# Kernel tuning notes

Measured on AMD Instinct MI355X. Metric: run time of the kernel, lower is better.

The kernel has to match this reference:

```python
import jax, jax.numpy as jnp
import numpy as np

FFT_SIZE = 1024
FRAME_LEN = 256   # stft is called with frame_length = hop_size = 256
FRAME_STEP = 128  # frame_length // 2 (stft default)
N_BINS = FFT_SIZE // 2 + 1
EPS = 1e-8
W_LOG = 1.0
W_LIN = 1.0


def _dft_weights():
    # periodic hann window (scipy get_window(..., fftbins=True))
    n = jnp.arange(FRAME_LEN, dtype=jnp.float32)
    win = 0.5 - 0.5 * jnp.cos(2.0 * jnp.pi * n / FRAME_LEN)
    lp = (FFT_SIZE - FRAME_LEN) // 2
    win = jnp.pad(win, (lp, FFT_SIZE - FRAME_LEN - lp))  # center-pad to n_fft
    # DFT matrix entries exp(-2*pi*i*k*f/n): use exact integer phase mod n_fft
    k = jnp.arange(FFT_SIZE, dtype=jnp.int32)[:, None]
    f = jnp.arange(N_BINS, dtype=jnp.int32)[None, :]
    theta = (-2.0 * jnp.pi / FFT_SIZE) * ((k * f) % FFT_SIZE).astype(jnp.float32)
    w_re = (jnp.cos(theta) * win[:, None])[:, None, :]  # [n_fft, 1, n_bins] (HIO)
    w_im = (jnp.sin(theta) * win[:, None])[:, None, :]
    return w_re, w_im


def _stft_mag(x, w_re, w_im):
    # pad='end' -> pad (0, n_fft - 1) along time
    sig = jnp.pad(x[:, :, None], ((0, 0), (0, FFT_SIZE - 1), (0, 0)))
    dn = ('NHC', 'HIO', 'NHC')
    re = jax.lax.conv_general_dilated(sig, w_re, [FRAME_STEP], 'VALID', dimension_numbers=dn)
    im = jax.lax.conv_general_dilated(sig, w_im, [FRAME_STEP], 'VALID', dimension_numbers=dn)
    # original indexes x_stft[-1]: magnitude of the LAST batch element only
    return jnp.sqrt(jnp.maximum(re[-1] ** 2 + im[-1] ** 2, EPS))  # [frames, n_bins]


def _loss(inp, tgt):
    w_re, w_im = _dft_weights()
    x_mag = _stft_mag(inp, w_re, w_im)
    y_mag = _stft_mag(tgt, w_re, w_im)
    log_mag = jnp.mean(jnp.abs(jnp.log(x_mag) - jnp.log(y_mag)))  # log_eps=0, log_fac=1, L1
    lin_mag = jnp.mean(jnp.abs(x_mag - y_mag))
    return W_LOG * log_mag + W_LIN * lin_mag  # w_sc=0, w_phs=0; 'mean' reduction on scalar is identity


def setup_inputs() -> dict:
    key = jax.random.key(0)
    k1, k2 = jax.random.split(key)
    B, T = 8, 524288
    return {
        'input': jax.random.normal(k1, (B, T), dtype=jnp.float32),
        'target': jax.random.normal(k2, (B, T), dtype=jnp.float32),
    }


def reference(input, target):
    return _loss(input, target)
```

## Files before the change

### kernel.cpp

```cpp
#include <hip/hip_runtime.h>
#include <hip/hip_bf16.h>


#define T_LEN    524288
#define WIN_OFF  384
#define EPSQ     1e-8f
#define INV_N    (1.0f / (4096.0f * 513.0f))
#define A2PI_1024 6.1359231515425647e-3f
#define A2PI_256  2.4543692606170259e-2f

typedef __attribute__((ext_vector_type(8))) __bf16 bf16x8;
typedef __attribute__((ext_vector_type(4))) float  f32x4;

union bfbits { __hip_bfloat16 hb; __bf16 b; unsigned short u; };
static __device__ __forceinline__ __bf16 f2bf(float f) {
    bfbits t; t.hb = __float2bfloat16(f); return t.b;
}

__global__ void prep(const float* __restrict__ x, const float* __restrict__ y,
                     __bf16* __restrict__ xb, __bf16* __restrict__ yb,
                     __bf16* __restrict__ bre, __bf16* __restrict__ bim)
{
    const int tid  = threadIdx.x;
    const int lane = tid & 63;
    const int wid  = blockIdx.x * 4 + (tid >> 6);

    if (wid < 4096) {
        const int sig = wid >> 11;
        const int chunk = wid & 2047;
        const int ft = chunk >> 3;
        const int kk = chunk & 7;
        const float* src = sig ? y : x;
        __bf16*      dst = sig ? yb : xb;
        const int frame = ft * 16 + (lane & 15);
        const int base  = frame * 128 + WIN_OFF + kk * 32 + (lane >> 4) * 8;
        bf16x8 v;
        if (base + 7 < T_LEN) {
            const float4 a0 = *(const float4*)(src + base);
            const float4 a1 = *(const float4*)(src + base + 4);
            v[0]=f2bf(a0.x); v[1]=f2bf(a0.y); v[2]=f2bf(a0.z); v[3]=f2bf(a0.w);
            v[4]=f2bf(a1.x); v[5]=f2bf(a1.y); v[6]=f2bf(a1.z); v[7]=f2bf(a1.w);
        } else {
            #pragma unroll
            for (int j = 0; j < 8; ++j) {
                const int idx = base + j;
                v[j] = f2bf(idx < T_LEN ? src[idx] : 0.f);
            }
        }
        *(bf16x8*)(dst + (size_t)chunk * 512 + lane * 8) = v;
    } else if (wid < 4096 + 256) {
        const int i  = wid - 4096;
        const int bt = i >> 3;
        const int kk = i & 7;
        const int bin = bt * 16 + (lane & 15);
        const int k0  = kk * 32 + (lane >> 4) * 8;
        bf16x8 vr, vi;
        #pragma unroll
        for (int j = 0; j < 8; ++j) {
            const int k = k0 + j;
            const float win = 0.5f - 0.5f * __cosf(A2PI_256 * (float)k);
            const int phase = ((WIN_OFF + k) * bin) & 1023;
            float s, c;
            __sincosf(-A2PI_1024 * (float)phase, &s, &c);
            vr[j] = f2bf(c * win);
            vi[j] = f2bf(s * win);
        }
        const size_t off = (size_t)i * 512 + lane * 8;
        *(bf16x8*)(bre + off) = vr;
        *(bf16x8*)(bim + off) = vi;
    }
}

__launch_bounds__(256, 4)
__global__ void stft_main(const __bf16* __restrict__ xb, const __bf16* __restrict__ yb,
                          const __bf16* __restrict__ bre, const __bf16* __restrict__ bim,
                          const float* __restrict__ x, const float* __restrict__ y,
                          float* __restrict__ partials)
{
    const int tid  = threadIdx.x;
    const int mb   = blockIdx.x & 127;
    const int nb   = blockIdx.x >> 7;

    const int lane = tid & 63;
    const int wv   = tid >> 6;
    const int wr   = wv >> 1;
    const int wc   = wv & 1;

    const int ft  = mb * 2 + wr;
    const int bt0 = nb * 4 + wc * 2;

    const __bf16* pax = xb  + (size_t)ft  * 4096 + lane * 8;
    const __bf16* pay = yb  + (size_t)ft  * 4096 + lane * 8;
    const __bf16* pr0 = bre + (size_t)bt0 * 4096 + lane * 8;
    const __bf16* pi0 = bim + (size_t)bt0 * 4096 + lane * 8;
    const __bf16* pr1 = pr0 + 4096;
    const __bf16* pi1 = pi0 + 4096;

    f32x4 axr[2], axi[2], ayr[2], ayi[2];
    #pragma unroll
    for (int ni = 0; ni < 2; ++ni) {
        axr[ni] = (f32x4)0.f; axi[ni] = (f32x4)0.f;
        ayr[ni] = (f32x4)0.f; ayi[ni] = (f32x4)0.f;
    }

    #pragma unroll 2
    for (int kk = 0; kk < 8; ++kk) {
        const int ko = kk * 512;
        const bf16x8 fax  = *(const bf16x8*)(pax + ko);
        const bf16x8 fay  = *(const bf16x8*)(pay + ko);
        const bf16x8 fbr0 = *(const bf16x8*)(pr0 + ko);
        const bf16x8 fbi0 = *(const bf16x8*)(pi0 + ko);
        const bf16x8 fbr1 = *(const bf16x8*)(pr1 + ko);
        const bf16x8 fbi1 = *(const bf16x8*)(pi1 + ko);

        axr[0] = __builtin_amdgcn_mfma_f32_16x16x32_bf16(fax, fbr0, axr[0], 0, 0, 0);
        axi[0] = __builtin_amdgcn_mfma_f32_16x16x32_bf16(fax, fbi0, axi[0], 0, 0, 0);
        ayr[0] = __builtin_amdgcn_mfma_f32_16x16x32_bf16(fay, fbr0, ayr[0], 0, 0, 0);
        ayi[0] = __builtin_amdgcn_mfma_f32_16x16x32_bf16(fay, fbi0, ayi[0], 0, 0, 0);
        axr[1] = __builtin_amdgcn_mfma_f32_16x16x32_bf16(fax, fbr1, axr[1], 0, 0, 0);
        axi[1] = __builtin_amdgcn_mfma_f32_16x16x32_bf16(fax, fbi1, axi[1], 0, 0, 0);
        ayr[1] = __builtin_amdgcn_mfma_f32_16x16x32_bf16(fay, fbr1, ayr[1], 0, 0, 0);
        ayi[1] = __builtin_amdgcn_mfma_f32_16x16x32_bf16(fay, fbi1, ayi[1], 0, 0, 0);
    }

    float sum = 0.f;
    #pragma unroll
    for (int ni = 0; ni < 2; ++ni)
        #pragma unroll
        for (int r = 0; r < 4; ++r) {
            const float xr = axr[ni][r], xi = axi[ni][r];
            const float yr = ayr[ni][r], yi = ayi[ni][r];
            const float xm = sqrtf(fmaxf(xr * xr + xi * xi, EPSQ));
            const float ym = sqrtf(fmaxf(yr * yr + yi * yi, EPSQ));
            sum += fabsf(__logf(xm) - __logf(ym)) + fabsf(xm - ym);
        }

    {
        float w4[4];
        #pragma unroll
        for (int j = 0; j < 4; ++j) {
            const int m = lane * 4 + j;
            const float win = 0.5f - 0.5f * __cosf(A2PI_256 * (float)m);
            w4[j] = (m & 1) ? -win : win;
        }
        const int frame = blockIdx.x * 4 + wv;
        const int base  = frame * 128 + WIN_OFF + lane * 4;
        float xr, yr;
        if (frame < 4092) {
            const float4 xv = *(const float4*)(x + base);
            const float4 yv = *(const float4*)(y + base);
            xr = xv.x * w4[0] + xv.y * w4[1] + xv.z * w4[2] + xv.w * w4[3];
            yr = yv.x * w4[0] + yv.y * w4[1] + yv.z * w4[2] + yv.w * w4[3];
        } else {
            xr = 0.f; yr = 0.f;
            #pragma unroll
            for (int j = 0; j < 4; ++j) {
                const int idx = base + j;
                if (idx < T_LEN) {
                    xr = fmaf(x[idx], w4[j], xr);
                    yr = fmaf(y[idx], w4[j], yr);
                }
            }
        }
        #pragma unroll
        for (int off = 32; off > 0; off >>= 1) {
            xr += __shfl_xor(xr, off, 64);
            yr += __shfl_xor(yr, off, 64);
        }
        if (lane == 0) {
            const float xm = sqrtf(fmaxf(xr * xr, EPSQ));
            const float ym = sqrtf(fmaxf(yr * yr, EPSQ));
            sum += fabsf(__logf(xm) - __logf(ym)) + fabsf(xm - ym);
        }
    }

    #pragma unroll
    for (int off = 32; off > 0; off >>= 1)
        sum += __shfl_down(sum, off, 64);

    __shared__ float red_s[4];
    if (lane == 0) red_s[wv] = sum;
    __syncthreads();
    if (tid == 0)
        partials[blockIdx.x] = red_s[0] + red_s[1] + red_s[2] + red_s[3];
}

__global__ void reduce_partials(const float* __restrict__ partials,
                                float* __restrict__ out)
{
    const int tid = threadIdx.x;
    float s = partials[tid] + partials[tid + 256]
            + partials[tid + 512] + partials[tid + 768];
    #pragma unroll
    for (int off = 32; off > 0; off >>= 1)
        s += __shfl_down(s, off, 64);

    __shared__ float red[4];
    if ((tid & 63) == 0) red[tid >> 6] = s;
    __syncthreads();
    if (tid == 0)
        out[0] = (red[0] + red[1] + red[2] + red[3]) * INV_N;
}

extern "C" void kernel_launch(void* const* d_in, const int* in_sizes, int n_in,
                              void* d_out, int out_size, void* d_ws, size_t ws_size,
                              hipStream_t stream) {
    const float* input  = (const float*)d_in[0];
    const float* target = (const float*)d_in[1];
    const float* x = input  + (size_t)7 * T_LEN;
    const float* y = target + (size_t)7 * T_LEN;

    char* ws = (char*)d_ws;
    __bf16* wsBre  = (__bf16*)(ws);
    __bf16* wsBim  = (__bf16*)(ws + 262144);
    __bf16* wsXb   = (__bf16*)(ws + 524288);
    __bf16* wsYb   = (__bf16*)(ws + 524288 + 2097152);
    float*  wsPart = (float*) (ws + 524288 + 4194304);

    prep<<<1088, 256, 0, stream>>>(x, y, wsXb, wsYb, wsBre, wsBim);
    stft_main<<<1024, 256, 0, stream>>>(wsXb, wsYb, wsBre, wsBim, x, y, wsPart);
    reduce_partials<<<1, 256, 0, stream>>>(wsPart, (float*)d_out);
}
```

Baseline: 24.24 us.

## Double per-wave frame tiles and fold final reduction into last-block atomic

Each wave now computes a 2x2 grid of 16x16 MFMA tiles (two frame tiles by two bin tiles), which halves the grid to 512 blocks and reuses each loaded fragment across twice as many MFMAs. The separate reduce_partials launch is removed: blocks publish partials with release stores, bump an atomic counter (reset in prep), and the last block sums all partials and writes the output. This is meant to cut global fragment traffic and one kernel launch. In exchange it raises register pressure (32 accumulators, occupancy hint dropped) and leaves fewer blocks to fill the GPU.

```diff
diff --git a/kernel.cpp b/kernel.cpp
--- a/kernel.cpp
+++ b/kernel.cpp
@@ -8,6 +8,7 @@
 #define INV_N    (1.0f / (4096.0f * 513.0f))
 #define A2PI_1024 6.1359231515425647e-3f
 #define A2PI_256  2.4543692606170259e-2f
+#define NBLK     512
 
 typedef __attribute__((ext_vector_type(8))) __bf16 bf16x8;
 typedef __attribute__((ext_vector_type(4))) float  f32x4;
@@ -19,11 +20,14 @@
 
 __global__ void prep(const float* __restrict__ x, const float* __restrict__ y,
                      __bf16* __restrict__ xb, __bf16* __restrict__ yb,
-                     __bf16* __restrict__ bre, __bf16* __restrict__ bim)
+                     __bf16* __restrict__ bre, __bf16* __restrict__ bim,
+                     unsigned* __restrict__ counter)
 {
     const int tid  = threadIdx.x;
     const int lane = tid & 63;
     const int wid  = blockIdx.x * 4 + (tid >> 6);
+
+    if (blockIdx.x == 0 && tid == 0) *counter = 0u;
 
     if (wid < 4096) {
         const int sig = wid >> 11;
@@ -71,69 +75,76 @@
     }
 }
 
-__launch_bounds__(256, 4)
+__launch_bounds__(256)
 __global__ void stft_main(const __bf16* __restrict__ xb, const __bf16* __restrict__ yb,
                           const __bf16* __restrict__ bre, const __bf16* __restrict__ bim,
                           const float* __restrict__ x, const float* __restrict__ y,
-                          float* __restrict__ partials)
+                          float* __restrict__ partials, unsigned* __restrict__ counter,
+                          float* __restrict__ out)
 {
     const int tid  = threadIdx.x;
-    const int mb   = blockIdx.x & 127;
-    const int nb   = blockIdx.x >> 7;
+    const int mb   = blockIdx.x & 63;
+    const int nb   = blockIdx.x >> 6;
 
     const int lane = tid & 63;
     const int wv   = tid >> 6;
     const int wr   = wv >> 1;
     const int wc   = wv & 1;
 
-    const int ft  = mb * 2 + wr;
+    const int ft0 = mb * 4 + wr * 2;
     const int bt0 = nb * 4 + wc * 2;
 
-    const __bf16* pax = xb  + (size_t)ft  * 4096 + lane * 8;
-    const __bf16* pay = yb  + (size_t)ft  * 4096 + lane * 8;
-    const __bf16* pr0 = bre + (size_t)bt0 * 4096 + lane * 8;
-    const __bf16* pi0 = bim + (size_t)bt0 * 4096 + lane * 8;
-    const __bf16* pr1 = pr0 + 4096;
-    const __bf16* pi1 = pi0 + 4096;
-
-    f32x4 axr[2], axi[2], ayr[2], ayi[2];
+    const __bf16* pax0 = xb  + (size_t)ft0 * 4096 + lane * 8;
+    const __bf16* pay0 = yb  + (size_t)ft0 * 4096 + lane * 8;
+    const __bf16* pbr0 = bre + (size_t)bt0 * 4096 + lane * 8;
+    const __bf16* pbi0 = bim + (size_t)bt0 * 4096 + lane * 8;
+
+    f32x4 axr[2][2], axi[2][2], ayr[2][2], ayi[2][2];
     #pragma unroll
-    for (int ni = 0; ni < 2; ++ni) {
-        axr[ni] = (f32x4)0.f; axi[ni] = (f32x4)0.f;
-        ayr[ni] = (f32x4)0.f; ayi[ni] = (f32x4)0.f;
-    }
+    for (int mi = 0; mi < 2; ++mi)
+        #pragma unroll
+        for (int ni = 0; ni < 2; ++ni) {
+            axr[mi][ni] = (f32x4)0.f; axi[mi][ni] = (f32x4)0.f;
+            ayr[mi][ni] = (f32x4)0.f; ayi[mi][ni] = (f32x4)0.f;
+        }
 
     #pragma unroll 2
     for (int kk = 0; kk < 8; ++kk) {
         const int ko = kk * 512;
-        const bf16x8 fax  = *(const bf16x8*)(pax + ko);
-        const bf16x8 fay  = *(const bf16x8*)(pay + ko);
-        const bf16x8 fbr0 = *(const bf16x8*)(pr0 + ko);
-        const bf16x8 fbi0 = *(const bf16x8*)(pi0 + ko);
-        const bf16x8 fbr1 = *(const bf16x8*)(pr1 + ko);
-        const bf16x8 fbi1 = *(const bf16x8*)(pi1 + ko);
-
-        axr[0] = __builtin_amdgcn_mfma_f32_16x16x32_bf16(fax, fbr0, axr[0], 0, 0, 0);
-        axi[0] = __builtin_amdgcn_mfma_f32_16x16x32_bf16(fax, fbi0, axi[0], 0, 0, 0);
-        ayr[0] = __builtin_amdgcn_mfma_f32_16x16x32_bf16(fay, fbr0, ayr[0], 0, 0, 0);
-        ayi[0] = __builtin_amdgcn_mfma_f32_16x16x32_bf16(fay, fbi0, ayi[0], 0, 0, 0);
-        axr[1] = __builtin_amdgcn_mfma_f32_16x16x32_bf16(fax, fbr1, axr[1], 0, 0, 0);
-        axi[1] = __builtin_amdgcn_mfma_f32_16x16x32_bf16(fax, fbi1, axi[1], 0, 0, 0);
-        ayr[1] = __builtin_amdgcn_mfma_f32_16x16x32_bf16(fay, fbr1, ayr[1], 0, 0, 0);
-        ayi[1] = __builtin_amdgcn_mfma_f32_16x16x32_bf16(fay, fbi1, ayi[1], 0, 0, 0);
+        bf16x8 fax[2], fay[2], fbr[2], fbi[2];
+        fax[0] = *(const bf16x8*)(pax0 + ko);
+        fax[1] = *(const bf16x8*)(pax0 + ko + 4096);
+        fay[0] = *(const bf16x8*)(pay0 + ko);
+        fay[1] = *(const bf16x8*)(pay0 + ko + 4096);
+        fbr[0] = *(const bf16x8*)(pbr0 + ko);
+        fbr[1] = *(const bf16x8*)(pbr0 + ko + 4096);
+        fbi[0] = *(const bf16x8*)(pbi0 + ko);
+        fbi[1] = *(const bf16x8*)(pbi0 + ko + 4096);
+
+        #pragma unroll
+        for (int mi = 0; mi < 2; ++mi)
+            #pragma unroll
+            for (int ni = 0; ni < 2; ++ni) {
+                axr[mi][ni] = __builtin_amdgcn_mfma_f32_16x16x32_bf16(fax[mi], fbr[ni], axr[mi][ni], 0, 0, 0);
+                axi[mi][ni] = __builtin_amdgcn_mfma_f32_16x16x32_bf16(fax[mi], fbi[ni], axi[mi][ni], 0, 0, 0);
+                ayr[mi][ni] = __builtin_amdgcn_mfma_f32_16x16x32_bf16(fay[mi], fbr[ni], ayr[mi][ni], 0, 0, 0);
+                ayi[mi][ni] = __builtin_amdgcn_mfma_f32_16x16x32_bf16(fay[mi], fbi[ni], ayi[mi][ni], 0, 0, 0);
+            }
     }
 
     float sum = 0.f;
     #pragma unroll
-    for (int ni = 0; ni < 2; ++ni)
-        #pragma unroll
-        for (int r = 0; r < 4; ++r) {
-            const float xr = axr[ni][r], xi = axi[ni][r];
-            const float yr = ayr[ni][r], yi = ayi[ni][r];
-            const float xm = sqrtf(fmaxf(xr * xr + xi * xi, EPSQ));
-            const float ym = sqrtf(fmaxf(yr * yr + yi * yi, EPSQ));
-            sum += fabsf(__logf(xm) - __logf(ym)) + fabsf(xm - ym);
-        }
+    for (int mi = 0; mi < 2; ++mi)
+        #pragma unroll
+        for (int ni = 0; ni < 2; ++ni)
+            #pragma unroll
+            for (int r = 0; r < 4; ++r) {
+                const float xr = axr[mi][ni][r], xi = axi[mi][ni][r];
+                const float yr = ayr[mi][ni][r], yi = ayi[mi][ni][r];
+                const float xm = sqrtf(fmaxf(xr * xr + xi * xi, EPSQ));
+                const float ym = sqrtf(fmaxf(yr * yr + yi * yi, EPSQ));
+                sum += fabsf(__logf(xm) - __logf(ym)) + fabsf(xm - ym);
+            }
 
     {
         float w4[4];
@@ -143,34 +154,37 @@
             const float win = 0.5f - 0.5f * __cosf(A2PI_256 * (float)m);
             w4[j] = (m & 1) ? -win : win;
         }
-        const int frame = blockIdx.x * 4 + wv;
-        const int base  = frame * 128 + WIN_OFF + lane * 4;
-        float xr, yr;
-        if (frame < 4092) {
-            const float4 xv = *(const float4*)(x + base);
-            const float4 yv = *(const float4*)(y + base);
-            xr = xv.x * w4[0] + xv.y * w4[1] + xv.z * w4[2] + xv.w * w4[3];
-            yr = yv.x * w4[0] + yv.y * w4[1] + yv.z * w4[2] + yv.w * w4[3];
-        } else {
-            xr = 0.f; yr = 0.f;
-            #pragma unroll
-            for (int j = 0; j < 4; ++j) {
-                const int idx = base + j;
-                if (idx < T_LEN) {
-                    xr = fmaf(x[idx], w4[j], xr);
-                    yr = fmaf(y[idx], w4[j], yr);
+        #pragma unroll
+        for (int e = 0; e < 2; ++e) {
+            const int frame = blockIdx.x * 8 + wv * 2 + e;
+            const int base  = frame * 128 + WIN_OFF + lane * 4;
+            float xr, yr;
+            if (frame < 4092) {
+                const float4 xv = *(const float4*)(x + base);
+                const float4 yv = *(const float4*)(y + base);
+                xr = xv.x * w4[0] + xv.y * w4[1] + xv.z * w4[2] + xv.w * w4[3];
+                yr = yv.x * w4[0] + yv.y * w4[1] + yv.z * w4[2] + yv.w * w4[3];
+            } else {
+                xr = 0.f; yr = 0.f;
+                #pragma unroll
+                for (int j = 0; j < 4; ++j) {
+                    const int idx = base + j;
+                    if (idx < T_LEN) {
+                        xr = fmaf(x[idx], w4[j], xr);
+                        yr = fmaf(y[idx], w4[j], yr);
+                    }
                 }
             }
-        }
-        #pragma unroll
-        for (int off = 32; off > 0; off >>= 1) {
-            xr += __shfl_xor(xr, off, 64);
-            yr += __shfl_xor(yr, off, 64);
-        }
-        if (lane == 0) {
-            const float xm = sqrtf(fmaxf(xr * xr, EPSQ));
-            const float ym = sqrtf(fmaxf(yr * yr, EPSQ));
-            sum += fabsf(__logf(xm) - __logf(ym)) + fabsf(xm - ym);
+            #pragma unroll
+            for (int off = 32; off > 0; off >>= 1) {
+                xr += __shfl_xor(xr, off, 64);
+                yr += __shfl_xor(yr, off, 64);
+            }
+            if (lane == 0) {
+                const float xm = sqrtf(fmaxf(xr * xr, EPSQ));
+                const float ym = sqrtf(fmaxf(yr * yr, EPSQ));
+                sum += fabsf(__logf(xm) - __logf(ym)) + fabsf(xm - ym);
+            }
         }
     }
 
@@ -179,27 +193,32 @@
         sum += __shfl_down(sum, off, 64);
 
     __shared__ float red_s[4];
+    __shared__ bool  amLast;
     if (lane == 0) red_s[wv] = sum;
     __syncthreads();
-    if (tid == 0)
-        partials[blockIdx.x] = red_s[0] + red_s[1] + red_s[2] + red_s[3];
-}
-
-__global__ void reduce_partials(const float* __restrict__ partials,
-                                float* __restrict__ out)
-{
-    const int tid = threadIdx.x;
-    float s = partials[tid] + partials[tid + 256]
-            + partials[tid + 512] + partials[tid + 768];
-    #pragma unroll
-    for (int off = 32; off > 0; off >>= 1)
-        s += __shfl_down(s, off, 64);
-
-    __shared__ float red[4];
-    if ((tid & 63) == 0) red[tid >> 6] = s;
+    if (tid == 0) {
+        const float p = red_s[0] + red_s[1] + red_s[2] + red_s[3];
+        __hip_atomic_store(&partials[blockIdx.x], p,
+                           __ATOMIC_RELEASE, __HIP_MEMORY_SCOPE_AGENT);
+        const unsigned old = __hip_atomic_fetch_add(counter, 1u,
+                           __ATOMIC_ACQ_REL, __HIP_MEMORY_SCOPE_AGENT);
+        amLast = (old == NBLK - 1);
+    }
     __syncthreads();
-    if (tid == 0)
-        out[0] = (red[0] + red[1] + red[2] + red[3]) * INV_N;
+
+    if (amLast) {
+        float s = __hip_atomic_load(&partials[tid],
+                      __ATOMIC_RELAXED, __HIP_MEMORY_SCOPE_AGENT)
+                + __hip_atomic_load(&partials[tid + 256],
+                      __ATOMIC_RELAXED, __HIP_MEMORY_SCOPE_AGENT);
+        #pragma unroll
+        for (int off = 32; off > 0; off >>= 1)
+            s += __shfl_down(s, off, 64);
+        if (lane == 0) red_s[wv] = s;
+        __syncthreads();
+        if (tid == 0)
+            out[0] = (red_s[0] + red_s[1] + red_s[2] + red_s[3]) * INV_N;
+    }
 }
 
 extern "C" void kernel_launch(void* const* d_in, const int* in_sizes, int n_in,
@@ -211,13 +230,14 @@
     const float* y = target + (size_t)7 * T_LEN;
 
     char* ws = (char*)d_ws;
-    __bf16* wsBre  = (__bf16*)(ws);
-    __bf16* wsBim  = (__bf16*)(ws + 262144);
-    __bf16* wsXb   = (__bf16*)(ws + 524288);
-    __bf16* wsYb   = (__bf16*)(ws + 524288 + 2097152);
-    float*  wsPart = (float*) (ws + 524288 + 4194304);
-
-    prep<<<1088, 256, 0, stream>>>(x, y, wsXb, wsYb, wsBre, wsBim);
-    stft_main<<<1024, 256, 0, stream>>>(wsXb, wsYb, wsBre, wsBim, x, y, wsPart);
-    reduce_partials<<<1, 256, 0, stream>>>(wsPart, (float*)d_out);
-}
+    __bf16*   wsBre  = (__bf16*)(ws);
+    __bf16*   wsBim  = (__bf16*)(ws + 262144);
+    __bf16*   wsXb   = (__bf16*)(ws + 524288);
+    __bf16*   wsYb   = (__bf16*)(ws + 524288 + 2097152);
+    float*    wsPart = (float*) (ws + 524288 + 4194304);
+    unsigned* wsCtr  = (unsigned*)(ws + 524288 + 4194304 + 2048);
+
+    prep<<<1088, 256, 0, stream>>>(x, y, wsXb, wsYb, wsBre, wsBim, wsCtr);
+    stft_main<<<NBLK, 256, 0, stream>>>(wsXb, wsYb, wsBre, wsBim, x, y,
+                                        wsPart, wsCtr, (float*)d_out);
+}
```

New measurement: 31.72 us. 1.31x slower.
